# Performance work log

Hardware: AMD Instinct MI355X
Metric: run time of the kernel (lower is better)

Reference implementation:

```python
import jax, jax.numpy as jnp
import numpy as np

EPS = 1e-7  # Keras backend epsilon


def setup_inputs() -> dict:
    key = jax.random.key(0)
    kx, ka, ke, kp = jax.random.split(key, 4)
    B, N, F, K_, C = 8, 2048, 128, 128, 128
    X = jax.random.normal(kx, (B, N, F), dtype=jnp.float32)
    Au = (jax.random.uniform(ka, (B, N, N)) < 0.05).astype(jnp.float32)
    A = jnp.maximum(Au, jnp.swapaxes(Au, -1, -2))
    W_emb = jax.random.normal(ke, (F, C), dtype=jnp.float32) * 0.1
    W_pool = jax.random.normal(kp, (F, K_), dtype=jnp.float32) * 0.1
    return {"X": X, "A": A, "W_emb": W_emb, "W_pool": W_pool}


def _diffpool(X, A, W_emb, W_pool):
    N = A.shape[-1]
    I = jnp.eye(N, dtype=A.dtype)
    A_ = A + I
    # symmetric normalization D^-1/2 (A+I) D^-1/2
    d = jax.lax.rsqrt(jnp.sum(A_, axis=-1))          # [B, N]
    fltr = A_ * d[..., :, None] * d[..., None, :]    # [B, N, N]

    Z = jnp.einsum('bnm,bmc->bnc', fltr, X @ W_emb)  # embedding GNN (no activation)
    S = jax.nn.softmax(jnp.einsum('bnm,bmk->bnk', fltr, X @ W_pool), axis=-1)  # [B, N, k]

    # link prediction loss: ||A - S S^T||_F per graph, mean over batch
    S_gram = jnp.einsum('bnk,bmk->bnm', S, S)
    LP_loss = jnp.mean(jnp.linalg.norm(A - S_gram, ord='fro', axis=(-1, -2)))

    # entropy loss on assignments
    entr = -jnp.sum(S * jnp.log(S + EPS), axis=-1)   # [B, N]
    entr_loss = jnp.mean(entr)

    X_pooled = jnp.einsum('bnk,bnc->bkc', S, Z)                  # S^T Z
    A_pooled = jnp.einsum('bnk,bnm,bml->bkl', S, A, S)           # S^T A S
    return X_pooled, A_pooled, S, LP_loss, entr_loss


def reference(X, A, W_emb, W_pool):
    return _diffpool(X, A, W_emb, W_pool)
```

## Files before the change

### kernel.cpp

```cpp
#include <hip/hip_runtime.h>
#include <math.h>

typedef __bf16 bf16x8 __attribute__((ext_vector_type(8)));
typedef float  f32x4  __attribute__((ext_vector_type(4)));
typedef unsigned short u16x4 __attribute__((ext_vector_type(4)));

#define DEVI __device__ __forceinline__

static constexpr int NB  = 8;
static constexpr int NN  = 2048;
static constexpr int NF  = 128;
static constexpr int NC2 = 256;
static constexpr int NSK = 16;

static constexpr int OUT_X0  = 0;
static constexpr int OUT_A0  = NB * 128 * 128;
static constexpr int OUT_S0  = OUT_A0 + NB * 128 * 128;
static constexpr int OUT_LP  = OUT_S0 + NB * NN * 128;
static constexpr int OUT_ENT = OUT_LP + 1;

DEVI unsigned short f2b(float f) {
  unsigned int u = __builtin_bit_cast(unsigned int, f);
  u += 0x7fffu + ((u >> 16) & 1u);
  return (unsigned short)(u >> 16);
}
DEVI float b2f(unsigned short h) {
  unsigned int u = ((unsigned int)h) << 16;
  return __builtin_bit_cast(float, u);
}
DEVI void load_lds16(const void* g, void* l) {
  __builtin_amdgcn_global_load_lds(
      (const __attribute__((address_space(1))) void*)g,
      (__attribute__((address_space(3))) void*)l, 16, 0, 0);
}
DEVI int swz(int row) { return (row >> 1) & 3; }

DEVI void stage_b128(const unsigned short* src, int ld, unsigned short* dst,
                     int k0, int tid) {
  const int wave = tid >> 6;
#pragma unroll
  for (int is = 0; is < 2; ++is) {
    const int row = is * 64 + (tid >> 2);
    const int c   = tid & 3;
    load_lds16(src + row * ld + k0 + ((c ^ swz(row)) << 3),
               dst + ((is * 256 + wave * 64) << 3));
  }
}
DEVI void stage_a64(const unsigned short* src, int ld, unsigned short* dst,
                    int k0, int tid) {
  const int wave = tid >> 6;
  const int row = tid >> 2, c = tid & 3;
  load_lds16(src + row * ld + k0 + ((c ^ swz(row)) << 3), dst + (wave << 9));
}

DEVI void gemm_core64(const unsigned short* Aop, int lda,
                      const unsigned short* Bop, int ldb, int ksteps,
                      unsigned short* lA0, unsigned short* lA1,
                      unsigned short* lB0, unsigned short* lB1,
                      int tid, f32x4 (&acc)[4][2]) {
  const int lane = tid & 63, wave = tid >> 6;
  const int l15 = lane & 15;
  const int sx = (lane >> 4) ^ ((l15 >> 1) & 3);
#pragma unroll
  for (int i = 0; i < 4; ++i) {
    acc[i][0] = (f32x4){0.f, 0.f, 0.f, 0.f};
    acc[i][1] = (f32x4){0.f, 0.f, 0.f, 0.f};
  }
  stage_a64(Aop, lda, lA0, 0, tid);
  stage_b128(Bop, ldb, lB0, 0, tid);
  __syncthreads();
  for (int kt = 0; kt < ksteps; ++kt) {
    unsigned short* curA = (kt & 1) ? lA1 : lA0;
    unsigned short* curB = (kt & 1) ? lB1 : lB0;
    if (kt + 1 < ksteps) {
      const int k0 = (kt + 1) * 32;
      stage_a64(Aop, lda, (kt & 1) ? lA0 : lA1, k0, tid);
      stage_b128(Bop, ldb, (kt & 1) ? lB0 : lB1, k0, tid);
    }
    bf16x8 af[4], bg[2];
#pragma unroll
    for (int i = 0; i < 4; ++i)
      af[i] = *(const bf16x8*)(curA + (((i * 16 + l15) * 4 + sx) << 3));
#pragma unroll
    for (int j = 0; j < 2; ++j)
      bg[j] = *(const bf16x8*)(curB + (((wave * 32 + j * 16 + l15) * 4 + sx) << 3));
#pragma unroll
    for (int i = 0; i < 4; ++i)
#pragma unroll
      for (int j = 0; j < 2; ++j)
        acc[i][j] = __builtin_amdgcn_mfma_f32_16x16x32_bf16(af[i], bg[j],
                                                            acc[i][j], 0, 0, 0);
    __syncthreads();
  }
}

DEVI void gemm_core128(const unsigned short* Aop, int lda,
                       const unsigned short* Bop, int ldb, int ksteps,
                       unsigned short* lA0, unsigned short* lA1,
                       unsigned short* lB0, unsigned short* lB1,
                       int tid, f32x4 (&acc)[4][4]) {
  const int lane = tid & 63, wave = tid >> 6;
  const int wr = wave >> 1, wc = wave & 1;
  const int l15 = lane & 15;
  const int sx = (lane >> 4) ^ ((l15 >> 1) & 3);
#pragma unroll
  for (int i = 0; i < 4; ++i)
#pragma unroll
    for (int j = 0; j < 4; ++j) acc[i][j] = (f32x4){0.f, 0.f, 0.f, 0.f};
  stage_b128(Aop, lda, lA0, 0, tid);
  stage_b128(Bop, ldb, lB0, 0, tid);
  __syncthreads();
  for (int kt = 0; kt < ksteps; ++kt) {
    unsigned short* curA = (kt & 1) ? lA1 : lA0;
    unsigned short* curB = (kt & 1) ? lB1 : lB0;
    if (kt + 1 < ksteps) {
      const int k0 = (kt + 1) * 32;
      stage_b128(Aop, lda, (kt & 1) ? lA0 : lA1, k0, tid);
      stage_b128(Bop, ldb, (kt & 1) ? lB0 : lB1, k0, tid);
    }
    bf16x8 af[4], bg[4];
#pragma unroll
    for (int i = 0; i < 4; ++i)
      af[i] = *(const bf16x8*)(curA + (((wr * 64 + i * 16 + l15) * 4 + sx) << 3));
#pragma unroll
    for (int j = 0; j < 4; ++j)
      bg[j] = *(const bf16x8*)(curB + (((wc * 64 + j * 16 + l15) * 4 + sx) << 3));
#pragma unroll
    for (int i = 0; i < 4; ++i)
#pragma unroll
      for (int j = 0; j < 4; ++j)
        acc[i][j] = __builtin_amdgcn_mfma_f32_16x16x32_bf16(af[i], bg[j],
                                                            acc[i][j], 0, 0, 0);
    __syncthreads();
  }
}

__global__ __launch_bounds__(256) void k_prep(const float* __restrict__ A,
                                              const float* __restrict__ X,
                                              const float* __restrict__ Wemb,
                                              const float* __restrict__ Wpool,
                                              unsigned short* __restrict__ AB,
                                              unsigned short* __restrict__ XB,
                                              unsigned short* __restrict__ WT,
                                              float* __restrict__ dvec,
                                              float* __restrict__ rsum) {
  const int blk = blockIdx.x, tid = threadIdx.x;
  if (blk < 4096) {
    const int row = blk * 4 + (tid >> 6);
    const int lane = tid & 63;
    const f32x4* src = (const f32x4*)(A + ((size_t)row << 11));
    u16x4* dst = (u16x4*)(AB + ((size_t)row << 11));
    float s = 0.f;
#pragma unroll
    for (int it = 0; it < 8; ++it) {
      f32x4 v = src[it * 64 + lane];
      s += v[0] + v[1] + v[2] + v[3];
      u16x4 o;
      o[0] = f2b(v[0]); o[1] = f2b(v[1]); o[2] = f2b(v[2]); o[3] = f2b(v[3]);
      dst[it * 64 + lane] = o;
    }
#pragma unroll
    for (int o2 = 32; o2; o2 >>= 1) s += __shfl_down(s, o2);
    if (lane == 0) { dvec[row] = rsqrtf(s + 1.f); rsum[row] = s; }
  } else if (blk < 4608) {
    const int i0 = (blk - 4096) * 1024 + tid;
    const f32x4* src = (const f32x4*)X;
    u16x4* dst = (u16x4*)XB;
#pragma unroll
    for (int it = 0; it < 4; ++it) {
      const int idx = i0 + it * 256;
      f32x4 v = src[idx];
      u16x4 o;
      o[0] = f2b(v[0]); o[1] = f2b(v[1]); o[2] = f2b(v[2]); o[3] = f2b(v[3]);
      dst[idx] = o;
    }
  } else {
    const int e = (blk - 4608) * 256 + tid;
    const int c = e >> 4, f0 = (e & 15) * 8;
    const float* W = (c < 128) ? Wemb : Wpool;
    const int cc = c & 127;
#pragma unroll
    for (int q = 0; q < 8; ++q)
      WT[c * 128 + f0 + q] = f2b(W[(f0 + q) * 128 + cc]);
  }
}

__global__ __launch_bounds__(256) void k_gemm_xw(const unsigned short* __restrict__ XB,
                                                 const unsigned short* __restrict__ WT,
                                                 const float* __restrict__ dvec,
                                                 unsigned short* __restrict__ VT) {
  __shared__ unsigned short lA[2][2048], lB[2][4096];
  const int mt = blockIdx.x, ct = blockIdx.y, tid = threadIdx.x;
  f32x4 acc[4][2];
  gemm_core64(XB + mt * 64 * NF, NF, WT + ct * 128 * NF, NF, NF / 32,
              lA[0], lA[1], lB[0], lB[1], tid, acc);
  const int lane = tid & 63, wave = tid >> 6;
  const int l15 = lane & 15, l4 = (lane >> 4) * 4;
#pragma unroll
  for (int i = 0; i < 4; ++i) {
    const int gr0 = mt * 64 + i * 16 + l4;
    const int b = gr0 >> 11, n0 = gr0 & 2047;
    const f32x4 dv = *(const f32x4*)(dvec + gr0);
#pragma unroll
    for (int j = 0; j < 2; ++j) {
      const int gc = ct * 128 + wave * 32 + j * 16 + l15;
      u16x4 pk;
#pragma unroll
      for (int r = 0; r < 4; ++r) pk[r] = f2b(acc[i][j][r] * dv[r]);
      *(u16x4*)(VT + (((size_t)(b * NC2 + gc)) << 11) + n0) = pk;
    }
  }
}

__global__ __launch_bounds__(256) void k_gemm_nv(const unsigned short* __restrict__ AB,
                                                 const unsigned short* __restrict__ VT,
                                                 const float* __restrict__ dvec,
                                                 unsigned short* __restrict__ YT,
                                                 float* __restrict__ out,
                                                 float* __restrict__ entv) {
  __shared__ unsigned short lA[2][2048], lB[2][4096];
  const int mt = blockIdx.x, ct = blockIdx.y, b = blockIdx.z, tid = threadIdx.x;
  const unsigned short* Aop = AB + ((size_t)b << 22) + (size_t)mt * 64 * NN;
  const unsigned short* Bop = VT + (((size_t)(b * NC2 + ct * 128)) << 11);
  f32x4 acc[4][2];
  gemm_core64(Aop, NN, Bop, NN, NN / 32, lA[0], lA[1], lB[0], lB[1], tid, acc);
  const int lane = tid & 63, wave = tid >> 6;
  const int l15 = lane & 15, l4g = lane >> 4, l4 = l4g * 4;
  f32x4 dv[4];
#pragma unroll
  for (int i = 0; i < 4; ++i)
    dv[i] = *(const f32x4*)(dvec + (b << 11) + mt * 64 + i * 16 + l4);
#pragma unroll
  for (int i = 0; i < 4; ++i) {
    const int n0 = mt * 64 + i * 16 + l4;
#pragma unroll
    for (int j = 0; j < 2; ++j) {
      const int c = ct * 128 + wave * 32 + j * 16 + l15;
      const u16x4 vv = *(const u16x4*)(VT + (((size_t)(b * NC2 + c)) << 11) + n0);
#pragma unroll
      for (int r = 0; r < 4; ++r)
        acc[i][j][r] = (acc[i][j][r] + b2f(vv[r])) * dv[i][r];
    }
  }
  if (ct == 0) {
#pragma unroll
    for (int i = 0; i < 4; ++i) {
      const int n0 = mt * 64 + i * 16 + l4;
#pragma unroll
      for (int j = 0; j < 2; ++j) {
        const int c = wave * 32 + j * 16 + l15;
        u16x4 pk;
#pragma unroll
        for (int r = 0; r < 4; ++r) pk[r] = f2b(acc[i][j][r]);
        *(u16x4*)(YT + (((size_t)(b * 384 + c)) << 11) + n0) = pk;
      }
    }
    return;
  }
  float* mbuf = (float*)lA;
  float* sbuf = mbuf + 256;
  float* tbuf = mbuf + 512;
  float* ebuf = mbuf + 768;
  float rm[4][4], rs[4][4], rt[4][4];
#pragma unroll
  for (int i = 0; i < 4; ++i)
#pragma unroll
    for (int r = 0; r < 4; ++r) {
      float m = fmaxf(acc[i][0][r], acc[i][1][r]);
#pragma unroll
      for (int off = 1; off < 16; off <<= 1) m = fmaxf(m, __shfl_xor(m, off));
      if (l15 == 0) mbuf[wave * 64 + i * 16 + l4 + r] = m;
    }
  __syncthreads();
#pragma unroll
  for (int i = 0; i < 4; ++i)
#pragma unroll
    for (int r = 0; r < 4; ++r) {
      const int row = i * 16 + l4 + r;
      rm[i][r] = fmaxf(fmaxf(mbuf[row], mbuf[64 + row]),
                       fmaxf(mbuf[128 + row], mbuf[192 + row]));
      rs[i][r] = 0.f; rt[i][r] = 0.f;
    }
#pragma unroll
  for (int i = 0; i < 4; ++i)
#pragma unroll
    for (int j = 0; j < 2; ++j)
#pragma unroll
      for (int r = 0; r < 4; ++r) {
        const float xm = acc[i][j][r] - rm[i][r];
        const float e = __expf(xm);
        acc[i][j][r] = e;
        rs[i][r] += e;
        rt[i][r] += xm * e;
      }
#pragma unroll
  for (int i = 0; i < 4; ++i)
#pragma unroll
    for (int r = 0; r < 4; ++r) {
      float s = rs[i][r], t = rt[i][r];
#pragma unroll
      for (int off = 1; off < 16; off <<= 1) {
        s += __shfl_xor(s, off); t += __shfl_xor(t, off);
      }
      if (l15 == 0) {
        sbuf[wave * 64 + i * 16 + l4 + r] = s;
        tbuf[wave * 64 + i * 16 + l4 + r] = t;
      }
    }
  __syncthreads();
  float ent = 0.f;
#pragma unroll
  for (int i = 0; i < 4; ++i)
#pragma unroll
    for (int r = 0; r < 4; ++r) {
      const int row = i * 16 + l4 + r;
      const float s = sbuf[row] + sbuf[64 + row] + sbuf[128 + row] + sbuf[192 + row];
      const float t = tbuf[row] + tbuf[64 + row] + tbuf[128 + row] + tbuf[192 + row];
      const float inv = 1.f / s;
      rs[i][r] = inv;
      ent += __logf(s) - t * inv;
    }
#pragma unroll
  for (int i = 0; i < 4; ++i) {
    const int n0 = mt * 64 + i * 16 + l4;
#pragma unroll
    for (int j = 0; j < 2; ++j) {
      const int c = wave * 32 + j * 16 + l15;
      u16x4 pk;
#pragma unroll
      for (int r = 0; r < 4; ++r) {
        const float sv = acc[i][j][r] * rs[i][r];
        pk[r] = f2b(sv);
        out[OUT_S0 + (((size_t)((b << 11) + n0 + r)) << 7) + c] = sv;
      }
      *(u16x4*)(YT + (((size_t)(b * 384 + 256 + c)) << 11) + n0) = pk;
    }
  }
  if (wave == 0 && l15 == 0) ebuf[l4g] = ent;
  __syncthreads();
  if (tid == 0)
    entv[b * 32 + mt] = ebuf[0] + ebuf[1] + ebuf[2] + ebuf[3];
}

__global__ __launch_bounds__(256) void k_gemm_as(const unsigned short* __restrict__ AB,
                                                 unsigned short* __restrict__ YT) {
  __shared__ unsigned short lA[2][2048], lB[2][4096];
  const int mt = blockIdx.x, b = blockIdx.z, tid = threadIdx.x;
  const unsigned short* Aop = AB + ((size_t)b << 22) + (size_t)mt * 64 * NN;
  const unsigned short* Bop = YT + (((size_t)(b * 384 + 256)) << 11);
  f32x4 acc[4][2];
  gemm_core64(Aop, NN, Bop, NN, NN / 32, lA[0], lA[1], lB[0], lB[1], tid, acc);
  const int lane = tid & 63, wave = tid >> 6;
  const int l15 = lane & 15, l4 = (lane >> 4) * 4;
#pragma unroll
  for (int i = 0; i < 4; ++i) {
    const int n0 = mt * 64 + i * 16 + l4;
#pragma unroll
    for (int j = 0; j < 2; ++j) {
      const int c = wave * 32 + j * 16 + l15;
      u16x4 pk;
#pragma unroll
      for (int r = 0; r < 4; ++r) pk[r] = f2b(acc[i][j][r]);
      *(u16x4*)(YT + (((size_t)(b * 384 + 128 + c)) << 11) + n0) = pk;
    }
  }
}

__global__ __launch_bounds__(256) void k_gemm_p(const unsigned short* __restrict__ YT,
                                                float* __restrict__ Pp) {
  __shared__ unsigned short lA[2][4096], lB[2][4096];
  const int ct = blockIdx.x, sk = blockIdx.y, b = blockIdx.z, tid = threadIdx.x;
  const unsigned short* Aop = YT + (((size_t)(b * 384 + 256)) << 11) + sk * 128;
  const unsigned short* Bop = YT + (((size_t)(b * 384 + ct * 128)) << 11) + sk * 128;
  f32x4 acc[4][4];
  gemm_core128(Aop, NN, Bop, NN, 4, lA[0], lA[1], lB[0], lB[1], tid, acc);
  const int lane = tid & 63, wave = tid >> 6;
  const int wr = wave >> 1, wc = wave & 1, l15 = lane & 15, l4 = (lane >> 4) * 4;
  float* dst = Pp + ((size_t)(sk * NB + b)) * 128 * 384;
#pragma unroll
  for (int i = 0; i < 4; ++i) {
    const int p0 = wr * 64 + i * 16 + l4;
#pragma unroll
    for (int j = 0; j < 4; ++j) {
      const int gc = ct * 128 + wc * 64 + j * 16 + l15;
#pragma unroll
      for (int r = 0; r < 4; ++r) dst[(p0 + r) * 384 + gc] = acc[i][j][r];
    }
  }
}

__global__ __launch_bounds__(256) void k_reduce_p(const float* __restrict__ Pp,
                                                  float* __restrict__ trp,
                                                  float* __restrict__ g2p,
                                                  float* __restrict__ out) {
  const int chunk = blockIdx.x, b = blockIdx.y, tid = threadIdx.x;
  const int e = chunk * 256 + tid;
  const int p = e / 384, c = e - p * 384;
  float s = 0.f;
#pragma unroll
  for (int sk = 0; sk < NSK; ++sk)
    s += Pp[((size_t)(sk * NB + b)) * (128 * 384) + e];
  float tr = 0.f, g2 = 0.f;
  if (c < 128) {
    out[OUT_X0 + ((size_t)(b * 128 + p)) * 128 + c] = s;
  } else if (c < 256) {
    out[OUT_A0 + ((size_t)(b * 128 + p)) * 128 + (c - 128)] = s;
    if (c - 128 == p) tr = s;
  } else {
    g2 = s * s;
  }
  __shared__ float rb[512];
  rb[tid] = tr; rb[256 + tid] = g2;
  __syncthreads();
  for (int o = 128; o; o >>= 1) {
    if (tid < o) { rb[tid] += rb[tid + o]; rb[256 + tid] += rb[256 + tid + o]; }
    __syncthreads();
  }
  if (tid == 0) { trp[b * 192 + chunk] = rb[0]; g2p[b * 192 + chunk] = rb[256]; }
}

__global__ __launch_bounds__(256) void k_lp(const float* __restrict__ rsum,
                                            const float* __restrict__ trp,
                                            const float* __restrict__ g2p,
                                            float* __restrict__ lpv) {
  const int b = blockIdx.x, tid = threadIdx.x;
  float nz = 0.f;
#pragma unroll
  for (int i = 0; i < 8; ++i) nz += rsum[(b << 11) + i * 256 + tid];
  float tr = (tid < 192) ? trp[b * 192 + tid] : 0.f;
  float g2 = (tid < 192) ? g2p[b * 192 + tid] : 0.f;
  __shared__ float rb[768];
  rb[tid] = nz; rb[256 + tid] = tr; rb[512 + tid] = g2;
  __syncthreads();
  for (int o = 128; o; o >>= 1) {
    if (tid < o) {
      rb[tid] += rb[tid + o];
      rb[256 + tid] += rb[256 + tid + o];
      rb[512 + tid] += rb[512 + tid + o];
    }
    __syncthreads();
  }
  if (tid == 0)
    lpv[b] = sqrtf(fmaxf(rb[0] - 2.f * rb[256] + rb[512], 0.f));
}

__global__ __launch_bounds__(256) void k_losses(const float* __restrict__ entv,
                                                const float* __restrict__ lpv,
                                                float* __restrict__ out) {
  const int tid = threadIdx.x;
  __shared__ float rb[256];
  rb[tid] = entv[tid];
  __syncthreads();
  for (int o = 128; o; o >>= 1) {
    if (tid < o) rb[tid] += rb[tid + o];
    __syncthreads();
  }
  if (tid == 0) {
    float lp = 0.f;
#pragma unroll
    for (int b = 0; b < 8; ++b) lp += lpv[b];
    out[OUT_LP] = 0.125f * lp;
    out[OUT_ENT] = rb[0] * (1.f / (NB * NN));
  }
}

extern "C" void kernel_launch(void* const* d_in, const int* in_sizes, int n_in,
                              void* d_out, int out_size, void* d_ws, size_t ws_size,
                              hipStream_t stream) {
  const float* X     = (const float*)d_in[0];
  const float* A     = (const float*)d_in[1];
  const float* Wemb  = (const float*)d_in[2];
  const float* Wpool = (const float*)d_in[3];
  float* out = (float*)d_out;

  char* ws = (char*)d_ws;
  size_t o = 0;
  unsigned short* AB = (unsigned short*)(ws + o); o += (size_t)NB * NN * NN * 2;
  unsigned short* XB = (unsigned short*)(ws + o); o += (size_t)NB * NN * NF * 2;
  unsigned short* WT = (unsigned short*)(ws + o); o += (size_t)NC2 * NF * 2;
  unsigned short* VT = (unsigned short*)(ws + o); o += (size_t)NB * NC2 * NN * 2;
  unsigned short* YT = (unsigned short*)(ws + o); o += (size_t)NB * 384 * NN * 2;
  float* Pp  = (float*)(ws + o); o += (size_t)NSK * NB * 128 * 384 * 4;
  float* dvec = (float*)(ws + o); o += (size_t)NB * NN * 4;
  float* rsum = (float*)(ws + o); o += (size_t)NB * NN * 4;
  float* trp  = (float*)(ws + o); o += (size_t)NB * 192 * 4;
  float* g2p  = (float*)(ws + o); o += (size_t)NB * 192 * 4;
  float* entv = (float*)(ws + o); o += 256 * 4;
  float* lpv  = (float*)(ws + o); o += NB * 4;

  k_prep    <<<dim3(4624), 256, 0, stream>>>(A, X, Wemb, Wpool, AB, XB, WT, dvec, rsum);
  k_gemm_xw <<<dim3(NB * NN / 64, 2), 256, 0, stream>>>(XB, WT, dvec, VT);
  k_gemm_nv <<<dim3(NN / 64, 2, NB), 256, 0, stream>>>(AB, VT, dvec, YT, out, entv);
  k_gemm_as <<<dim3(NN / 64, 1, NB), 256, 0, stream>>>(AB, YT);
  k_gemm_p  <<<dim3(3, NSK, NB), 256, 0, stream>>>(YT, Pp);
  k_reduce_p<<<dim3(192, NB), 256, 0, stream>>>(Pp, trp, g2p, out);
  k_lp      <<<dim3(NB), 256, 0, stream>>>(rsum, trp, g2p, lpv);
  k_losses  <<<1, 256, 0, stream>>>(entv, lpv, out);
}
```

Baseline: 308.7 us.

## Fuse pipeline into persistent megakernel with hierarchical grid barriers

Replaces eight separate kernel launches with one persistent 512-block kernel that runs each stage in turn, separated by software grid barriers built from atomic counters in workspace. The N×V GEMM is also merged so each block computes both the 128-column embedding half and the 128-column pooling half with a 256-wide B tile. This avoids per-launch overhead and tail gaps between stages. In exchange, stages with fewer than 512 blocks leave blocks idle, the A-conversion stage runs with only 512 blocks, every block must be co-resident or the barriers deadlock, and the barrier counters need a separate zeroing launch.

```diff
diff --git a/kernel.cpp b/kernel.cpp
--- a/kernel.cpp
+++ b/kernel.cpp
@@ -12,6 +12,7 @@
 static constexpr int NF  = 128;
 static constexpr int NC2 = 256;
 static constexpr int NSK = 16;
+static constexpr int NBLK = 512;
 
 static constexpr int OUT_X0  = 0;
 static constexpr int OUT_A0  = NB * 128 * 128;
@@ -19,6 +20,9 @@
 static constexpr int OUT_LP  = OUT_S0 + NB * NN * 128;
 static constexpr int OUT_ENT = OUT_LP + 1;
 
+static constexpr int BAR_STRIDE = 65 * 32;
+static constexpr int BAR_UINTS  = 6 * BAR_STRIDE;
+
 DEVI unsigned short f2b(float f) {
   unsigned int u = __builtin_bit_cast(unsigned int, f);
   u += 0x7fffu + ((u >> 16) & 1u);
@@ -35,29 +39,55 @@
 }
 DEVI int swz(int row) { return (row >> 1) & 3; }
 
-DEVI void stage_b128(const unsigned short* src, int ld, unsigned short* dst,
-                     int k0, int tid) {
-  const int wave = tid >> 6;
-#pragma unroll
-  for (int is = 0; is < 2; ++is) {
-    const int row = is * 64 + (tid >> 2);
-    const int c   = tid & 3;
-    load_lds16(src + row * ld + k0 + ((c ^ swz(row)) << 3),
-               dst + ((is * 256 + wave * 64) << 3));
-  }
-}
+DEVI void gbar(unsigned* bar, int phase, int tid, int bid) {
+  __syncthreads();
+  if (tid == 0) {
+    __threadfence();
+    unsigned* base = bar + phase * BAR_STRIDE;
+    if (atomicAdd(base + ((bid >> 3) << 5), 1u) == 7u)
+      atomicAdd(base + 2048, 1u);
+    while (__hip_atomic_load(base + 2048, __ATOMIC_RELAXED,
+                             __HIP_MEMORY_SCOPE_AGENT) < 64u)
+      __builtin_amdgcn_s_sleep(2);
+    __threadfence();
+  }
+  __syncthreads();
+}
+
 DEVI void stage_a64(const unsigned short* src, int ld, unsigned short* dst,
                     int k0, int tid) {
   const int wave = tid >> 6;
   const int row = tid >> 2, c = tid & 3;
-  load_lds16(src + row * ld + k0 + ((c ^ swz(row)) << 3), dst + (wave << 9));
-}
-
-DEVI void gemm_core64(const unsigned short* Aop, int lda,
-                      const unsigned short* Bop, int ldb, int ksteps,
-                      unsigned short* lA0, unsigned short* lA1,
-                      unsigned short* lB0, unsigned short* lB1,
-                      int tid, f32x4 (&acc)[4][2]) {
+  load_lds16(src + (size_t)row * ld + k0 + ((c ^ swz(row)) << 3), dst + (wave << 9));
+}
+DEVI void stage_b128(const unsigned short* src, int ld, unsigned short* dst,
+                     int k0, int tid) {
+  const int wave = tid >> 6;
+#pragma unroll
+  for (int is = 0; is < 2; ++is) {
+    const int row = is * 64 + (tid >> 2);
+    const int c   = tid & 3;
+    load_lds16(src + (size_t)row * ld + k0 + ((c ^ swz(row)) << 3),
+               dst + ((is * 256 + wave * 64) << 3));
+  }
+}
+DEVI void stage_b256(const unsigned short* src, int ld, unsigned short* dst,
+                     int k0, int tid) {
+  const int wave = tid >> 6;
+#pragma unroll
+  for (int is = 0; is < 4; ++is) {
+    const int row = is * 64 + (tid >> 2);
+    const int c   = tid & 3;
+    load_lds16(src + (size_t)row * ld + k0 + ((c ^ swz(row)) << 3),
+               dst + ((is * 256 + wave * 64) << 3));
+  }
+}
+
+DEVI void core64(const unsigned short* Aop, int lda,
+                 const unsigned short* Bop, int ldb, int ksteps,
+                 unsigned short* lA0, unsigned short* lA1,
+                 unsigned short* lB0, unsigned short* lB1,
+                 int tid, f32x4 (&acc)[4][2]) {
   const int lane = tid & 63, wave = tid >> 6;
   const int l15 = lane & 15;
   const int sx = (lane >> 4) ^ ((l15 >> 1) & 3);
@@ -94,11 +124,11 @@
   }
 }
 
-DEVI void gemm_core128(const unsigned short* Aop, int lda,
-                       const unsigned short* Bop, int ldb, int ksteps,
-                       unsigned short* lA0, unsigned short* lA1,
-                       unsigned short* lB0, unsigned short* lB1,
-                       int tid, f32x4 (&acc)[4][4]) {
+DEVI void core128(const unsigned short* Aop, int lda,
+                  const unsigned short* Bop, int ldb, int ksteps,
+                  unsigned short* lA0, unsigned short* lA1,
+                  unsigned short* lB0, unsigned short* lB1,
+                  int tid, f32x4 (&acc)[4][4]) {
   const int lane = tid & 63, wave = tid >> 6;
   const int wr = wave >> 1, wc = wave & 1;
   const int l15 = lane & 15;
@@ -135,114 +165,153 @@
   }
 }
 
-__global__ __launch_bounds__(256) void k_prep(const float* __restrict__ A,
-                                              const float* __restrict__ X,
-                                              const float* __restrict__ Wemb,
-                                              const float* __restrict__ Wpool,
-                                              unsigned short* __restrict__ AB,
-                                              unsigned short* __restrict__ XB,
-                                              unsigned short* __restrict__ WT,
-                                              float* __restrict__ dvec,
-                                              float* __restrict__ rsum) {
-  const int blk = blockIdx.x, tid = threadIdx.x;
-  if (blk < 4096) {
-    const int row = blk * 4 + (tid >> 6);
-    const int lane = tid & 63;
-    const f32x4* src = (const f32x4*)(A + ((size_t)row << 11));
-    u16x4* dst = (u16x4*)(AB + ((size_t)row << 11));
-    float s = 0.f;
-#pragma unroll
-    for (int it = 0; it < 8; ++it) {
-      f32x4 v = src[it * 64 + lane];
-      s += v[0] + v[1] + v[2] + v[3];
-      u16x4 o;
-      o[0] = f2b(v[0]); o[1] = f2b(v[1]); o[2] = f2b(v[2]); o[3] = f2b(v[3]);
-      dst[it * 64 + lane] = o;
-    }
-#pragma unroll
-    for (int o2 = 32; o2; o2 >>= 1) s += __shfl_down(s, o2);
-    if (lane == 0) { dvec[row] = rsqrtf(s + 1.f); rsum[row] = s; }
-  } else if (blk < 4608) {
-    const int i0 = (blk - 4096) * 1024 + tid;
-    const f32x4* src = (const f32x4*)X;
-    u16x4* dst = (u16x4*)XB;
-#pragma unroll
-    for (int it = 0; it < 4; ++it) {
-      const int idx = i0 + it * 256;
-      f32x4 v = src[idx];
-      u16x4 o;
-      o[0] = f2b(v[0]); o[1] = f2b(v[1]); o[2] = f2b(v[2]); o[3] = f2b(v[3]);
-      dst[idx] = o;
-    }
-  } else {
-    const int e = (blk - 4608) * 256 + tid;
-    const int c = e >> 4, f0 = (e & 15) * 8;
-    const float* W = (c < 128) ? Wemb : Wpool;
-    const int cc = c & 127;
-#pragma unroll
-    for (int q = 0; q < 8; ++q)
-      WT[c * 128 + f0 + q] = f2b(W[(f0 + q) * 128 + cc]);
-  }
-}
-
-__global__ __launch_bounds__(256) void k_gemm_xw(const unsigned short* __restrict__ XB,
-                                                 const unsigned short* __restrict__ WT,
-                                                 const float* __restrict__ dvec,
-                                                 unsigned short* __restrict__ VT) {
-  __shared__ unsigned short lA[2][2048], lB[2][4096];
-  const int mt = blockIdx.x, ct = blockIdx.y, tid = threadIdx.x;
-  f32x4 acc[4][2];
-  gemm_core64(XB + mt * 64 * NF, NF, WT + ct * 128 * NF, NF, NF / 32,
-              lA[0], lA[1], lB[0], lB[1], tid, acc);
-  const int lane = tid & 63, wave = tid >> 6;
-  const int l15 = lane & 15, l4 = (lane >> 4) * 4;
-#pragma unroll
-  for (int i = 0; i < 4; ++i) {
-    const int gr0 = mt * 64 + i * 16 + l4;
-    const int b = gr0 >> 11, n0 = gr0 & 2047;
-    const f32x4 dv = *(const f32x4*)(dvec + gr0);
-#pragma unroll
-    for (int j = 0; j < 2; ++j) {
-      const int gc = ct * 128 + wave * 32 + j * 16 + l15;
-      u16x4 pk;
-#pragma unroll
-      for (int r = 0; r < 4; ++r) pk[r] = f2b(acc[i][j][r] * dv[r]);
-      *(u16x4*)(VT + (((size_t)(b * NC2 + gc)) << 11) + n0) = pk;
-    }
-  }
-}
-
-__global__ __launch_bounds__(256) void k_gemm_nv(const unsigned short* __restrict__ AB,
-                                                 const unsigned short* __restrict__ VT,
-                                                 const float* __restrict__ dvec,
-                                                 unsigned short* __restrict__ YT,
-                                                 float* __restrict__ out,
-                                                 float* __restrict__ entv) {
-  __shared__ unsigned short lA[2][2048], lB[2][4096];
-  const int mt = blockIdx.x, ct = blockIdx.y, b = blockIdx.z, tid = threadIdx.x;
-  const unsigned short* Aop = AB + ((size_t)b << 22) + (size_t)mt * 64 * NN;
-  const unsigned short* Bop = VT + (((size_t)(b * NC2 + ct * 128)) << 11);
-  f32x4 acc[4][2];
-  gemm_core64(Aop, NN, Bop, NN, NN / 32, lA[0], lA[1], lB[0], lB[1], tid, acc);
+__global__ __launch_bounds__(256) void k_zero(unsigned* __restrict__ bar) {
+  const int idx = blockIdx.x * 256 + threadIdx.x;
+  if (idx < BAR_UINTS) bar[idx] = 0u;
+}
+
+__global__ __launch_bounds__(256, 2) void k_mega(
+    const float* __restrict__ A, const float* __restrict__ X,
+    const float* __restrict__ Wemb, const float* __restrict__ Wpool,
+    float* __restrict__ out,
+    unsigned short* __restrict__ AB, unsigned short* __restrict__ XB,
+    unsigned short* __restrict__ WT, unsigned short* __restrict__ VT,
+    unsigned short* __restrict__ YT, float* __restrict__ Pp,
+    float* __restrict__ dvec, float* __restrict__ rsum,
+    float* __restrict__ trp, float* __restrict__ g2p,
+    float* __restrict__ entv, unsigned* __restrict__ bar) {
+  __shared__ __align__(16) unsigned char smem[40960];
+  unsigned short* sm16 = (unsigned short*)smem;
+  float* smf = (float*)smem;
+  const int bid = blockIdx.x, tid = threadIdx.x;
   const int lane = tid & 63, wave = tid >> 6;
   const int l15 = lane & 15, l4g = lane >> 4, l4 = l4g * 4;
-  f32x4 dv[4];
-#pragma unroll
-  for (int i = 0; i < 4; ++i)
-    dv[i] = *(const f32x4*)(dvec + (b << 11) + mt * 64 + i * 16 + l4);
-#pragma unroll
-  for (int i = 0; i < 4; ++i) {
-    const int n0 = mt * 64 + i * 16 + l4;
-#pragma unroll
-    for (int j = 0; j < 2; ++j) {
-      const int c = ct * 128 + wave * 32 + j * 16 + l15;
-      const u16x4 vv = *(const u16x4*)(VT + (((size_t)(b * NC2 + c)) << 11) + n0);
-#pragma unroll
-      for (int r = 0; r < 4; ++r)
-        acc[i][j][r] = (acc[i][j][r] + b2f(vv[r])) * dv[i][r];
-    }
-  }
-  if (ct == 0) {
+
+  {
+#pragma unroll 1
+    for (int q = 0; q < 8; ++q) {
+      const int row = bid * 32 + wave * 8 + q;
+      const f32x4* src = (const f32x4*)(A + ((size_t)row << 11));
+      u16x4* dst = (u16x4*)(AB + ((size_t)row << 11));
+      float s = 0.f;
+#pragma unroll
+      for (int it = 0; it < 8; ++it) {
+        f32x4 v = src[it * 64 + lane];
+        s += v[0] + v[1] + v[2] + v[3];
+        u16x4 o2;
+        o2[0] = f2b(v[0]); o2[1] = f2b(v[1]); o2[2] = f2b(v[2]); o2[3] = f2b(v[3]);
+        dst[it * 64 + lane] = o2;
+      }
+#pragma unroll
+      for (int o = 32; o; o >>= 1) s += __shfl_down(s, o);
+      if (lane == 0) { dvec[row] = rsqrtf(s + 1.f); rsum[row] = s; }
+    }
+    {
+      const int i0 = bid * 1024 + tid;
+      const f32x4* src = (const f32x4*)X;
+      u16x4* dst = (u16x4*)XB;
+#pragma unroll
+      for (int it = 0; it < 4; ++it) {
+        f32x4 v = src[i0 + it * 256];
+        u16x4 o2;
+        o2[0] = f2b(v[0]); o2[1] = f2b(v[1]); o2[2] = f2b(v[2]); o2[3] = f2b(v[3]);
+        dst[i0 + it * 256] = o2;
+      }
+    }
+    if (bid < 16) {
+      const int e = bid * 256 + tid;
+      const int c = e >> 4, f0 = (e & 15) * 8;
+      const float* W = (c < 128) ? Wemb : Wpool;
+      const int cc = c & 127;
+#pragma unroll
+      for (int q = 0; q < 8; ++q)
+        WT[c * 128 + f0 + q] = f2b(W[(f0 + q) * 128 + cc]);
+    }
+  }
+  gbar(bar, 0, tid, bid);
+
+  {
+    const int mt = bid >> 1, ct = bid & 1;
+    unsigned short* lA0 = sm16, *lA1 = sm16 + 2048;
+    unsigned short* lB0 = sm16 + 4096, *lB1 = sm16 + 8192;
+    f32x4 acc[4][2];
+    core64(XB + mt * 64 * NF, NF, WT + ct * 128 * NF, NF, NF / 32,
+           lA0, lA1, lB0, lB1, tid, acc);
+#pragma unroll
+    for (int i = 0; i < 4; ++i) {
+      const int gr0 = mt * 64 + i * 16 + l4;
+      const int b = gr0 >> 11, n0 = gr0 & 2047;
+      const f32x4 dv = *(const f32x4*)(dvec + gr0);
+#pragma unroll
+      for (int j = 0; j < 2; ++j) {
+        const int gc = ct * 128 + wave * 32 + j * 16 + l15;
+        u16x4 pk;
+#pragma unroll
+        for (int r = 0; r < 4; ++r) pk[r] = f2b(acc[i][j][r] * dv[r]);
+        *(u16x4*)(VT + (((size_t)(b * NC2 + gc)) << 11) + n0) = pk;
+      }
+    }
+  }
+  gbar(bar, 1, tid, bid);
+
+  if (bid < 256) {
+    const int mt = bid & 31, b = bid >> 5;
+    const unsigned short* Aop = AB + ((size_t)b << 22) + (size_t)mt * 64 * NN;
+    const unsigned short* Bop = VT + (((size_t)(b * NC2)) << 11);
+    unsigned short* lA0 = sm16, *lA1 = sm16 + 2048;
+    unsigned short* lB0 = sm16 + 4096, *lB1 = sm16 + 12288;
+    const int sx = (lane >> 4) ^ ((l15 >> 1) & 3);
+    f32x4 acc[4][4];
+#pragma unroll
+    for (int i = 0; i < 4; ++i)
+#pragma unroll
+      for (int j = 0; j < 4; ++j) acc[i][j] = (f32x4){0.f, 0.f, 0.f, 0.f};
+    stage_a64(Aop, NN, lA0, 0, tid);
+    stage_b256(Bop, NN, lB0, 0, tid);
+    __syncthreads();
+    for (int kt = 0; kt < 64; ++kt) {
+      unsigned short* curA = (kt & 1) ? lA1 : lA0;
+      unsigned short* curB = (kt & 1) ? lB1 : lB0;
+      if (kt + 1 < 64) {
+        const int k0 = (kt + 1) * 32;
+        stage_a64(Aop, NN, (kt & 1) ? lA0 : lA1, k0, tid);
+        stage_b256(Bop, NN, (kt & 1) ? lB0 : lB1, k0, tid);
+      }
+      bf16x8 af[4], bg[4];
+#pragma unroll
+      for (int i = 0; i < 4; ++i)
+        af[i] = *(const bf16x8*)(curA + (((i * 16 + l15) * 4 + sx) << 3));
+#pragma unroll
+      for (int j = 0; j < 4; ++j) {
+        const int row = (j < 2) ? (wave * 32 + j * 16 + l15)
+                                : (128 + wave * 32 + (j - 2) * 16 + l15);
+        bg[j] = *(const bf16x8*)(curB + ((row * 4 + sx) << 3));
+      }
+#pragma unroll
+      for (int i = 0; i < 4; ++i)
+#pragma unroll
+        for (int j = 0; j < 4; ++j)
+          acc[i][j] = __builtin_amdgcn_mfma_f32_16x16x32_bf16(af[i], bg[j],
+                                                              acc[i][j], 0, 0, 0);
+      __syncthreads();
+    }
+    f32x4 dv[4];
+#pragma unroll
+    for (int i = 0; i < 4; ++i)
+      dv[i] = *(const f32x4*)(dvec + (b << 11) + mt * 64 + i * 16 + l4);
+#pragma unroll
+    for (int i = 0; i < 4; ++i) {
+      const int n0 = mt * 64 + i * 16 + l4;
+#pragma unroll
+      for (int j = 0; j < 4; ++j) {
+        const int vrow = (j < 2) ? (wave * 32 + j * 16 + l15)
+                                 : (128 + wave * 32 + (j - 2) * 16 + l15);
+        const u16x4 vv = *(const u16x4*)(VT + (((size_t)(b * NC2 + vrow)) << 11) + n0);
+#pragma unroll
+        for (int r = 0; r < 4; ++r)
+          acc[i][j][r] = (acc[i][j][r] + b2f(vv[r])) * dv[i][r];
+      }
+    }
 #pragma unroll
     for (int i = 0; i < 4; ++i) {
       const int n0 = mt * 64 + i * 16 + l4;
@@ -255,212 +324,207 @@
         *(u16x4*)(YT + (((size_t)(b * 384 + c)) << 11) + n0) = pk;
       }
     }
-    return;
-  }
-  float* mbuf = (float*)lA;
-  float* sbuf = mbuf + 256;
-  float* tbuf = mbuf + 512;
-  float* ebuf = mbuf + 768;
-  float rm[4][4], rs[4][4], rt[4][4];
-#pragma unroll
-  for (int i = 0; i < 4; ++i)
-#pragma unroll
-    for (int r = 0; r < 4; ++r) {
-      float m = fmaxf(acc[i][0][r], acc[i][1][r]);
-#pragma unroll
-      for (int off = 1; off < 16; off <<= 1) m = fmaxf(m, __shfl_xor(m, off));
-      if (l15 == 0) mbuf[wave * 64 + i * 16 + l4 + r] = m;
-    }
-  __syncthreads();
-#pragma unroll
-  for (int i = 0; i < 4; ++i)
-#pragma unroll
-    for (int r = 0; r < 4; ++r) {
-      const int row = i * 16 + l4 + r;
-      rm[i][r] = fmaxf(fmaxf(mbuf[row], mbuf[64 + row]),
-                       fmaxf(mbuf[128 + row], mbuf[192 + row]));
-      rs[i][r] = 0.f; rt[i][r] = 0.f;
-    }
-#pragma unroll
-  for (int i = 0; i < 4; ++i)
-#pragma unroll
-    for (int j = 0; j < 2; ++j)
+    float* mbuf = smf;
+    float* sbuf = smf + 256;
+    float* tbuf = smf + 512;
+    float* ebuf = smf + 768;
+    float rm[4][4], rs[4][4], rt[4][4];
+#pragma unroll
+    for (int i = 0; i < 4; ++i)
 #pragma unroll
       for (int r = 0; r < 4; ++r) {
-        const float xm = acc[i][j][r] - rm[i][r];
-        const float e = __expf(xm);
-        acc[i][j][r] = e;
-        rs[i][r] += e;
-        rt[i][r] += xm * e;
-      }
-#pragma unroll
-  for (int i = 0; i < 4; ++i)
-#pragma unroll
-    for (int r = 0; r < 4; ++r) {
-      float s = rs[i][r], t = rt[i][r];
-#pragma unroll
-      for (int off = 1; off < 16; off <<= 1) {
-        s += __shfl_xor(s, off); t += __shfl_xor(t, off);
-      }
-      if (l15 == 0) {
-        sbuf[wave * 64 + i * 16 + l4 + r] = s;
-        tbuf[wave * 64 + i * 16 + l4 + r] = t;
-      }
-    }
-  __syncthreads();
-  float ent = 0.f;
-#pragma unroll
-  for (int i = 0; i < 4; ++i)
-#pragma unroll
-    for (int r = 0; r < 4; ++r) {
-      const int row = i * 16 + l4 + r;
-      const float s = sbuf[row] + sbuf[64 + row] + sbuf[128 + row] + sbuf[192 + row];
-      const float t = tbuf[row] + tbuf[64 + row] + tbuf[128 + row] + tbuf[192 + row];
-      const float inv = 1.f / s;
-      rs[i][r] = inv;
-      ent += __logf(s) - t * inv;
-    }
-#pragma unroll
-  for (int i = 0; i < 4; ++i) {
-    const int n0 = mt * 64 + i * 16 + l4;
-#pragma unroll
-    for (int j = 0; j < 2; ++j) {
-      const int c = wave * 32 + j * 16 + l15;
-      u16x4 pk;
+        float m = fmaxf(acc[i][2][r], acc[i][3][r]);
+#pragma unroll
+        for (int off = 1; off < 16; off <<= 1) m = fmaxf(m, __shfl_xor(m, off));
+        if (l15 == 0) mbuf[wave * 64 + i * 16 + l4 + r] = m;
+      }
+    __syncthreads();
+#pragma unroll
+    for (int i = 0; i < 4; ++i)
 #pragma unroll
       for (int r = 0; r < 4; ++r) {
-        const float sv = acc[i][j][r] * rs[i][r];
-        pk[r] = f2b(sv);
-        out[OUT_S0 + (((size_t)((b << 11) + n0 + r)) << 7) + c] = sv;
-      }
-      *(u16x4*)(YT + (((size_t)(b * 384 + 256 + c)) << 11) + n0) = pk;
-    }
-  }
-  if (wave == 0 && l15 == 0) ebuf[l4g] = ent;
-  __syncthreads();
-  if (tid == 0)
-    entv[b * 32 + mt] = ebuf[0] + ebuf[1] + ebuf[2] + ebuf[3];
-}
-
-__global__ __launch_bounds__(256) void k_gemm_as(const unsigned short* __restrict__ AB,
-                                                 unsigned short* __restrict__ YT) {
-  __shared__ unsigned short lA[2][2048], lB[2][4096];
-  const int mt = blockIdx.x, b = blockIdx.z, tid = threadIdx.x;
-  const unsigned short* Aop = AB + ((size_t)b << 22) + (size_t)mt * 64 * NN;
-  const unsigned short* Bop = YT + (((size_t)(b * 384 + 256)) << 11);
-  f32x4 acc[4][2];
-  gemm_core64(Aop, NN, Bop, NN, NN / 32, lA[0], lA[1], lB[0], lB[1], tid, acc);
-  const int lane = tid & 63, wave = tid >> 6;
-  const int l15 = lane & 15, l4 = (lane >> 4) * 4;
-#pragma unroll
-  for (int i = 0; i < 4; ++i) {
-    const int n0 = mt * 64 + i * 16 + l4;
-#pragma unroll
-    for (int j = 0; j < 2; ++j) {
-      const int c = wave * 32 + j * 16 + l15;
-      u16x4 pk;
-#pragma unroll
-      for (int r = 0; r < 4; ++r) pk[r] = f2b(acc[i][j][r]);
-      *(u16x4*)(YT + (((size_t)(b * 384 + 128 + c)) << 11) + n0) = pk;
-    }
-  }
-}
-
-__global__ __launch_bounds__(256) void k_gemm_p(const unsigned short* __restrict__ YT,
-                                                float* __restrict__ Pp) {
-  __shared__ unsigned short lA[2][4096], lB[2][4096];
-  const int ct = blockIdx.x, sk = blockIdx.y, b = blockIdx.z, tid = threadIdx.x;
-  const unsigned short* Aop = YT + (((size_t)(b * 384 + 256)) << 11) + sk * 128;
-  const unsigned short* Bop = YT + (((size_t)(b * 384 + ct * 128)) << 11) + sk * 128;
-  f32x4 acc[4][4];
-  gemm_core128(Aop, NN, Bop, NN, 4, lA[0], lA[1], lB[0], lB[1], tid, acc);
-  const int lane = tid & 63, wave = tid >> 6;
-  const int wr = wave >> 1, wc = wave & 1, l15 = lane & 15, l4 = (lane >> 4) * 4;
-  float* dst = Pp + ((size_t)(sk * NB + b)) * 128 * 384;
-#pragma unroll
-  for (int i = 0; i < 4; ++i) {
-    const int p0 = wr * 64 + i * 16 + l4;
-#pragma unroll
-    for (int j = 0; j < 4; ++j) {
-      const int gc = ct * 128 + wc * 64 + j * 16 + l15;
-#pragma unroll
-      for (int r = 0; r < 4; ++r) dst[(p0 + r) * 384 + gc] = acc[i][j][r];
-    }
-  }
-}
-
-__global__ __launch_bounds__(256) void k_reduce_p(const float* __restrict__ Pp,
-                                                  float* __restrict__ trp,
-                                                  float* __restrict__ g2p,
-                                                  float* __restrict__ out) {
-  const int chunk = blockIdx.x, b = blockIdx.y, tid = threadIdx.x;
-  const int e = chunk * 256 + tid;
-  const int p = e / 384, c = e - p * 384;
-  float s = 0.f;
-#pragma unroll
-  for (int sk = 0; sk < NSK; ++sk)
-    s += Pp[((size_t)(sk * NB + b)) * (128 * 384) + e];
-  float tr = 0.f, g2 = 0.f;
-  if (c < 128) {
-    out[OUT_X0 + ((size_t)(b * 128 + p)) * 128 + c] = s;
-  } else if (c < 256) {
-    out[OUT_A0 + ((size_t)(b * 128 + p)) * 128 + (c - 128)] = s;
-    if (c - 128 == p) tr = s;
-  } else {
-    g2 = s * s;
-  }
-  __shared__ float rb[512];
-  rb[tid] = tr; rb[256 + tid] = g2;
-  __syncthreads();
-  for (int o = 128; o; o >>= 1) {
-    if (tid < o) { rb[tid] += rb[tid + o]; rb[256 + tid] += rb[256 + tid + o]; }
-    __syncthreads();
-  }
-  if (tid == 0) { trp[b * 192 + chunk] = rb[0]; g2p[b * 192 + chunk] = rb[256]; }
-}
-
-__global__ __launch_bounds__(256) void k_lp(const float* __restrict__ rsum,
-                                            const float* __restrict__ trp,
-                                            const float* __restrict__ g2p,
-                                            float* __restrict__ lpv) {
-  const int b = blockIdx.x, tid = threadIdx.x;
-  float nz = 0.f;
-#pragma unroll
-  for (int i = 0; i < 8; ++i) nz += rsum[(b << 11) + i * 256 + tid];
-  float tr = (tid < 192) ? trp[b * 192 + tid] : 0.f;
-  float g2 = (tid < 192) ? g2p[b * 192 + tid] : 0.f;
-  __shared__ float rb[768];
-  rb[tid] = nz; rb[256 + tid] = tr; rb[512 + tid] = g2;
-  __syncthreads();
-  for (int o = 128; o; o >>= 1) {
-    if (tid < o) {
-      rb[tid] += rb[tid + o];
-      rb[256 + tid] += rb[256 + tid + o];
-      rb[512 + tid] += rb[512 + tid + o];
-    }
-    __syncthreads();
-  }
-  if (tid == 0)
-    lpv[b] = sqrtf(fmaxf(rb[0] - 2.f * rb[256] + rb[512], 0.f));
-}
-
-__global__ __launch_bounds__(256) void k_losses(const float* __restrict__ entv,
-                                                const float* __restrict__ lpv,
-                                                float* __restrict__ out) {
-  const int tid = threadIdx.x;
-  __shared__ float rb[256];
-  rb[tid] = entv[tid];
-  __syncthreads();
-  for (int o = 128; o; o >>= 1) {
-    if (tid < o) rb[tid] += rb[tid + o];
-    __syncthreads();
-  }
-  if (tid == 0) {
+        const int row = i * 16 + l4 + r;
+        rm[i][r] = fmaxf(fmaxf(mbuf[row], mbuf[64 + row]),
+                         fmaxf(mbuf[128 + row], mbuf[192 + row]));
+        rs[i][r] = 0.f; rt[i][r] = 0.f;
+      }
+#pragma unroll
+    for (int i = 0; i < 4; ++i)
+#pragma unroll
+      for (int j = 2; j < 4; ++j)
+#pragma unroll
+        for (int r = 0; r < 4; ++r) {
+          const float xm = acc[i][j][r] - rm[i][r];
+          const float e = __expf(xm);
+          acc[i][j][r] = e;
+          rs[i][r] += e;
+          rt[i][r] += xm * e;
+        }
+#pragma unroll
+    for (int i = 0; i < 4; ++i)
+#pragma unroll
+      for (int r = 0; r < 4; ++r) {
+        float s = rs[i][r], t = rt[i][r];
+#pragma unroll
+        for (int off = 1; off < 16; off <<= 1) {
+          s += __shfl_xor(s, off); t += __shfl_xor(t, off);
+        }
+        if (l15 == 0) {
+          sbuf[wave * 64 + i * 16 + l4 + r] = s;
+          tbuf[wave * 64 + i * 16 + l4 + r] = t;
+        }
+      }
+    __syncthreads();
+    float ent = 0.f;
+#pragma unroll
+    for (int i = 0; i < 4; ++i)
+#pragma unroll
+      for (int r = 0; r < 4; ++r) {
+        const int row = i * 16 + l4 + r;
+        const float s = sbuf[row] + sbuf[64 + row] + sbuf[128 + row] + sbuf[192 + row];
+        const float t = tbuf[row] + tbuf[64 + row] + tbuf[128 + row] + tbuf[192 + row];
+        const float inv = 1.f / s;
+        rs[i][r] = inv;
+        ent += __logf(s) - t * inv;
+      }
+#pragma unroll
+    for (int i = 0; i < 4; ++i) {
+      const int n0 = mt * 64 + i * 16 + l4;
+#pragma unroll
+      for (int j = 2; j < 4; ++j) {
+        const int cs = wave * 32 + (j - 2) * 16 + l15;
+        u16x4 pk;
+#pragma unroll
+        for (int r = 0; r < 4; ++r) {
+          const float sv = acc[i][j][r] * rs[i][r];
+          pk[r] = f2b(sv);
+          out[OUT_S0 + (((size_t)((b << 11) + n0 + r)) << 7) + cs] = sv;
+        }
+        *(u16x4*)(YT + (((size_t)(b * 384 + 256 + cs)) << 11) + n0) = pk;
+      }
+    }
+    if (wave == 0 && l15 == 0) ebuf[l4g] = ent;
+    __syncthreads();
+    if (tid == 0)
+      entv[b * 32 + mt] = ebuf[0] + ebuf[1] + ebuf[2] + ebuf[3];
+  }
+  gbar(bar, 2, tid, bid);
+
+  if (bid < 256) {
+    const int mt = bid & 31, b = bid >> 5;
+    unsigned short* lA0 = sm16, *lA1 = sm16 + 2048;
+    unsigned short* lB0 = sm16 + 4096, *lB1 = sm16 + 8192;
+    f32x4 acc[4][2];
+    core64(AB + ((size_t)b << 22) + (size_t)mt * 64 * NN, NN,
+           YT + (((size_t)(b * 384 + 256)) << 11), NN, NN / 32,
+           lA0, lA1, lB0, lB1, tid, acc);
+#pragma unroll
+    for (int i = 0; i < 4; ++i) {
+      const int n0 = mt * 64 + i * 16 + l4;
+#pragma unroll
+      for (int j = 0; j < 2; ++j) {
+        const int c = wave * 32 + j * 16 + l15;
+        u16x4 pk;
+#pragma unroll
+        for (int r = 0; r < 4; ++r) pk[r] = f2b(acc[i][j][r]);
+        *(u16x4*)(YT + (((size_t)(b * 384 + 128 + c)) << 11) + n0) = pk;
+      }
+    }
+  }
+  gbar(bar, 3, tid, bid);
+
+  if (bid < 384) {
+    const int ct = bid % 3, u = bid / 3;
+    const int sk = u & 15, b = u >> 4;
+    unsigned short* lA0 = sm16, *lA1 = sm16 + 4096;
+    unsigned short* lB0 = sm16 + 8192, *lB1 = sm16 + 12288;
+    f32x4 acc[4][4];
+    core128(YT + (((size_t)(b * 384 + 256)) << 11) + sk * 128, NN,
+            YT + (((size_t)(b * 384 + ct * 128)) << 11) + sk * 128, NN, 4,
+            lA0, lA1, lB0, lB1, tid, acc);
+    const int wr = wave >> 1, wc = wave & 1;
+    float* dst = Pp + ((size_t)(sk * NB + b)) * 128 * 384;
+#pragma unroll
+    for (int i = 0; i < 4; ++i) {
+      const int p0 = wr * 64 + i * 16 + l4;
+#pragma unroll
+      for (int j = 0; j < 4; ++j) {
+        const int gc = ct * 128 + wc * 64 + j * 16 + l15;
+#pragma unroll
+        for (int r = 0; r < 4; ++r) dst[(p0 + r) * 384 + gc] = acc[i][j][r];
+      }
+    }
+  }
+  gbar(bar, 4, tid, bid);
+
+  {
+#pragma unroll 1
+    for (int rep = 0; rep < 3; ++rep) {
+      __syncthreads();
+      const int ci = bid + rep * NBLK;
+      const int chunk = ci % 192, b = ci / 192;
+      const int e = chunk * 256 + tid;
+      const int p = e / 384, c = e - p * 384;
+      float s = 0.f;
+#pragma unroll
+      for (int sk = 0; sk < NSK; ++sk)
+        s += Pp[((size_t)(sk * NB + b)) * (128 * 384) + e];
+      float tr = 0.f, g2 = 0.f;
+      if (c < 128) {
+        out[OUT_X0 + ((size_t)(b * 128 + p)) * 128 + c] = s;
+      } else if (c < 256) {
+        out[OUT_A0 + ((size_t)(b * 128 + p)) * 128 + (c - 128)] = s;
+        if (c - 128 == p) tr = s;
+      } else {
+        g2 = s * s;
+      }
+      smf[tid] = tr; smf[256 + tid] = g2;
+      __syncthreads();
+      for (int o = 128; o; o >>= 1) {
+        if (tid < o) { smf[tid] += smf[tid + o]; smf[256 + tid] += smf[256 + tid + o]; }
+        __syncthreads();
+      }
+      if (tid == 0) { trp[b * 192 + chunk] = smf[0]; g2p[b * 192 + chunk] = smf[256]; }
+    }
+  }
+  gbar(bar, 5, tid, bid);
+
+  if (bid == 0) {
     float lp = 0.f;
-#pragma unroll
-    for (int b = 0; b < 8; ++b) lp += lpv[b];
-    out[OUT_LP] = 0.125f * lp;
-    out[OUT_ENT] = rb[0] * (1.f / (NB * NN));
+#pragma unroll 1
+    for (int b = 0; b < 8; ++b) {
+      float nz = 0.f;
+#pragma unroll
+      for (int i = 0; i < 8; ++i) nz += rsum[(b << 11) + i * 256 + tid];
+      float tr = (tid < 192) ? trp[b * 192 + tid] : 0.f;
+      float g2 = (tid < 192) ? g2p[b * 192 + tid] : 0.f;
+      __syncthreads();
+      smf[tid] = nz; smf[256 + tid] = tr; smf[512 + tid] = g2;
+      __syncthreads();
+      for (int o = 128; o; o >>= 1) {
+        if (tid < o) {
+          smf[tid] += smf[tid + o];
+          smf[256 + tid] += smf[256 + tid + o];
+          smf[512 + tid] += smf[512 + tid + o];
+        }
+        __syncthreads();
+      }
+      if (tid == 0)
+        lp += sqrtf(fmaxf(smf[0] - 2.f * smf[256] + smf[512], 0.f));
+      __syncthreads();
+    }
+    float e = entv[tid];
+    __syncthreads();
+    smf[tid] = e;
+    __syncthreads();
+    for (int o = 128; o; o >>= 1) {
+      if (tid < o) smf[tid] += smf[tid + o];
+      __syncthreads();
+    }
+    if (tid == 0) {
+      out[OUT_LP] = 0.125f * lp;
+      out[OUT_ENT] = smf[0] * (1.f / (NB * NN));
+    }
   }
 }
 
@@ -486,14 +550,9 @@
   float* trp  = (float*)(ws + o); o += (size_t)NB * 192 * 4;
   float* g2p  = (float*)(ws + o); o += (size_t)NB * 192 * 4;
   float* entv = (float*)(ws + o); o += 256 * 4;
-  float* lpv  = (float*)(ws + o); o += NB * 4;
-
-  k_prep    <<<dim3(4624), 256, 0, stream>>>(A, X, Wemb, Wpool, AB, XB, WT, dvec, rsum);
-  k_gemm_xw <<<dim3(NB * NN / 64, 2), 256, 0, stream>>>(XB, WT, dvec, VT);
-  k_gemm_nv <<<dim3(NN / 64, 2, NB), 256, 0, stream>>>(AB, VT, dvec, YT, out, entv);
-  k_gemm_as <<<dim3(NN / 64, 1, NB), 256, 0, stream>>>(AB, YT);
-  k_gemm_p  <<<dim3(3, NSK, NB), 256, 0, stream>>>(YT, Pp);
-  k_reduce_p<<<dim3(192, NB), 256, 0, stream>>>(Pp, trp, g2p, out);
-  k_lp      <<<dim3(NB), 256, 0, stream>>>(rsum, trp, g2p, lpv);
-  k_losses  <<<1, 256, 0, stream>>>(entv, lpv, out);
-}
+  unsigned* bar = (unsigned*)(ws + o); o += BAR_UINTS * 4;
+
+  k_zero<<<dim3((BAR_UINTS + 255) / 256), 256, 0, stream>>>(bar);
+  k_mega<<<dim3(NBLK), 256, 0, stream>>>(A, X, Wemb, Wpool, out, AB, XB, WT, VT,
+                                         YT, Pp, dvec, rsum, trp, g2p, entv, bar);
+}
```

Result: slower. 506.1 us (+64.0%).
